# Optimization experiments

Measured on AMD Instinct MI355X. Metric: run time of the kernel, lower is better.

Reference implementation:

```python
import jax, jax.numpy as jnp
import numpy as np

D_MODEL, N_STATE, L_MAX, BATCH = 256, 64, 2048, 16

def _to_c(x):
    return jax.lax.complex(x[..., 0], x[..., 1])

def setup_inputs() -> dict:
    key = jax.random.key(0)
    k_u, k_ct_r, k_ct_i, k_step = jax.random.split(key, 4)
    n, d = N_STATE, D_MODEL
    # --- HiPPO DPLR init (numpy, matches torch hippo_dplr) ---
    P = np.sqrt(1.0 + 2.0 * np.arange(1, n + 1, dtype=np.float64))
    A = np.tril(np.outer(P, P)) - np.diag(np.arange(1, n + 1, dtype=np.float64))
    A = -A
    p = 0.5 * np.sqrt(2.0 * np.arange(1, n + 1, dtype=np.float64) + 1.0)
    Ap = (A + np.outer(p, p)).astype(np.complex64)
    lam, V = np.linalg.eig(Ap)
    p_rot = V.conj().T @ p.astype(np.complex64)
    p_ri = np.stack([p_rot.real, p_rot.imag], -1).astype(np.float32)          # (n,2)
    lambda_ri = np.stack([lam.real, lam.imag], -1).astype(np.float32)         # (n,2)
    # --- B init: sqrt(2k+1), repeated over channels, zero imag ---
    B_r = np.sqrt(2.0 * np.arange(1, n + 1) + 1.0).astype(np.float32)
    B_ri = np.stack([np.tile(B_r, (d, 1)), np.zeros((d, n), np.float32)], -1) # (d,n,2)
    # --- Ct: xavier-normal complex ---
    std = float(np.sqrt(2.0 / (d + n)))
    Ct_r = jax.random.normal(k_ct_r, (d, n), jnp.float32) * (std / np.sqrt(2.0))
    Ct_i = jax.random.normal(k_ct_i, (d, n), jnp.float32) * (std / np.sqrt(2.0))
    Ct_ri = jnp.stack([Ct_r, Ct_i], -1)                                        # (d,n,2)
    Dp = jnp.ones((1, 1, d), jnp.float32)
    log_step = jax.random.uniform(k_step, (d,), jnp.float32) * (
        np.log(0.1) - np.log(0.001)) + np.log(0.001)
    u = jax.random.normal(k_u, (BATCH, L_MAX, d), jnp.float32)
    return {"u": u, "p_ri": jnp.asarray(p_ri), "lambda_ri": jnp.asarray(lambda_ri),
            "B_ri": jnp.asarray(B_ri), "Ct_ri": Ct_ri, "Dp": Dp, "log_step": log_step}

def reference(u, p_ri, lambda_ri, B_ri, Ct_ri, Dp, log_step):
    p = _to_c(p_ri)          # (n,)
    lam = _to_c(lambda_ri)   # (n,)
    B = _to_c(B_ri)          # (d,n)
    Ct = _to_c(Ct_ri)        # (d,n)
    L = u.shape[1]
    omega = jnp.exp(2j * jnp.pi * jnp.arange(L) / L).astype(jnp.complex64)  # (L,)
    step = jnp.exp(log_step)                                               # (d,)
    g = (2.0 / step)[:, None] * ((1.0 - omega) / (1.0 + omega))[None, :]   # (d,L)
    c = 2.0 / (1.0 + omega)                                                # (L,)
    inv = 1.0 / (g[:, :, None] - lam[None, None, :])                       # (d,L,n)
    k00 = jnp.einsum('dn,dln->dl', Ct.conj() * B, inv)
    k01 = jnp.einsum('dn,dln->dl', Ct.conj() * p[None, :], inv)
    k10 = jnp.einsum('dn,dln->dl', p.conj()[None, :] * B, inv)
    k11 = jnp.einsum('n,dln->dl', p.conj() * p, inv)
    at_roots = c[None, :] * (k00 - k01 * k10 / (1.0 + k11))                # (d,L)
    out = jnp.fft.ifft(at_roots, n=L, axis=-1)
    order = jnp.concatenate([jnp.zeros((1,), jnp.int32), jnp.arange(L - 1, 0, -1)])
    K = out[:, order].real[None]                                           # (1,d,L)
    # causal FFT convolution
    ud = jnp.fft.rfft(jnp.pad(u, ((0, 0), (0, L), (0, 0))), axis=1)        # (B,L+1,d)
    Kd = jnp.fft.rfft(jnp.pad(K, ((0, 0), (0, 0), (0, L))), axis=-1)       # (1,d,L+1)
    y = jnp.fft.irfft(jnp.transpose(ud, (0, 2, 1)) * Kd, axis=-1)[..., :L]
    y = jnp.transpose(y, (0, 2, 1)).astype(u.dtype)                        # (B,L,d)
    return y + Dp * u
```

## Files before the change

### kernel.cpp

```cpp
#include <hip/hip_runtime.h>
#include <math.h>

#define LLEN   2048
#define NFFT   4096
#define DMODEL 256
#define NSTATE 64
#define NBATCH 16
#define PI_F   3.14159265358979323846f

#define PADIDX(a) ((a) + ((a) >> 4))
#define LDSN2 (LLEN + (LLEN >> 4))
#define KSTRIDE 2056

#define SWZIDX(a) ((a) ^ (((a) >> 4) & 15))

__device__ inline float frcp(float x) { return __builtin_amdgcn_rcpf(x); }

#define RADIX4(ar0,ai0,ar1,ai1,ar2,ai2,ar3,ai3,S) do {                      \
    float s0r=(ar0)+(ar2), s0i=(ai0)+(ai2);                                 \
    float s1r=(ar0)-(ar2), s1i=(ai0)-(ai2);                                 \
    float s2r=(ar1)+(ar3), s2i=(ai1)+(ai3);                                 \
    float s3r=(ar1)-(ar3), s3i=(ai1)-(ai3);                                 \
    (ar0)=s0r+s2r; (ai0)=s0i+s2i;                                           \
    (ar2)=s0r-s2r; (ai2)=s0i-s2i;                                           \
    (ar1)=s1r-(S)*s3i; (ai1)=s1i+(S)*s3r;                                   \
    (ar3)=s1r+(S)*s3i; (ai3)=s1i-(S)*s3r;                                   \
} while (0)

template<int SIGN>
__device__ inline void dft16_tail(float xr[16], float xi[16]) {
    const float S = (float)SIGN;
    const float C1 = 0.9238795325112867f, S1 = 0.3826834323650898f;
    const float C2 = 0.7071067811865476f;
#define TW(idx, wr_, wi_) { float tr = xr[idx]*(wr_) - xi[idx]*(wi_);       \
    xi[idx] = xr[idx]*(wi_) + xi[idx]*(wr_); xr[idx] = tr; }
    TW(5,  C1,  S*S1);
    TW(6,  C2,  S*C2);
    TW(7,  S1,  S*C1);
    TW(9,  C2,  S*C2);
    TW(10, 0.f, S);
    TW(11, -C2, S*C2);
    TW(13, S1,  S*C1);
    TW(14, -C2, S*C2);
    TW(15, -C1, -S*S1);
#undef TW
    RADIX4(xr[0],xi[0],  xr[1],xi[1],  xr[2],xi[2],  xr[3],xi[3],  S);
    RADIX4(xr[4],xi[4],  xr[5],xi[5],  xr[6],xi[6],  xr[7],xi[7],  S);
    RADIX4(xr[8],xi[8],  xr[9],xi[9],  xr[10],xi[10],xr[11],xi[11],S);
    RADIX4(xr[12],xi[12],xr[13],xi[13],xr[14],xi[14],xr[15],xi[15],S);
}

template<int SIGN>
__device__ inline void dft16(float xr[16], float xi[16]) {
    const float S = (float)SIGN;
    RADIX4(xr[0],xi[0], xr[4],xi[4], xr[8],xi[8],  xr[12],xi[12], S);
    RADIX4(xr[1],xi[1], xr[5],xi[5], xr[9],xi[9],  xr[13],xi[13], S);
    RADIX4(xr[2],xi[2], xr[6],xi[6], xr[10],xi[10],xr[14],xi[14], S);
    RADIX4(xr[3],xi[3], xr[7],xi[7], xr[11],xi[11],xr[15],xi[15], S);
    dft16_tail<SIGN>(xr, xi);
}

template<int SIGN>
__device__ inline void dft16z(float xr[16], float xi[16]) {
    const float S = (float)SIGN;
#define RAD4Z(r0,i0,r1,i1,r2,i2,r3,i3) do {                                 \
    const float a0r=(r0), a0i=(i0), a1r=(r1), a1i=(i1);                     \
    (r0)=a0r+a1r;     (i0)=a0i+a1i;                                         \
    (r2)=a0r-a1r;     (i2)=a0i-a1i;                                         \
    (r1)=a0r-S*a1i;   (i1)=a0i+S*a1r;                                       \
    (r3)=a0r+S*a1i;   (i3)=a0i-S*a1r;                                       \
} while (0)
    RAD4Z(xr[0],xi[0], xr[4],xi[4], xr[8],xi[8],  xr[12],xi[12]);
    RAD4Z(xr[1],xi[1], xr[5],xi[5], xr[9],xi[9],  xr[13],xi[13]);
    RAD4Z(xr[2],xi[2], xr[6],xi[6], xr[10],xi[10],xr[14],xi[14]);
    RAD4Z(xr[3],xi[3], xr[7],xi[7], xr[11],xi[11],xr[15],xi[15]);
#undef RAD4Z
    dft16_tail<SIGN>(xr, xi);
}

template<int SIGN>
__device__ inline void dft8(float xr[8], float xi[8]) {
    const float S = (float)SIGN;
    const float C2 = 0.7071067811865476f;
    RADIX4(xr[0],xi[0], xr[2],xi[2], xr[4],xi[4], xr[6],xi[6], S);
    RADIX4(xr[1],xi[1], xr[3],xi[3], xr[5],xi[5], xr[7],xi[7], S);
    { float tr = xr[3]*C2 - xi[3]*(S*C2); xi[3] = xr[3]*(S*C2) + xi[3]*C2; xr[3] = tr; }
    { float tr = -S*xi[5]; xi[5] = S*xr[5]; xr[5] = tr; }
    { float tr = xr[7]*(-C2) - xi[7]*(S*C2); xi[7] = xr[7]*(S*C2) + xi[7]*(-C2); xr[7] = tr; }
    float br[8], bi[8];
#pragma unroll
    for (int k = 0; k < 4; ++k) {
        br[k]   = xr[2*k] + xr[2*k+1]; bi[k]   = xi[2*k] + xi[2*k+1];
        br[k+4] = xr[2*k] - xr[2*k+1]; bi[k+4] = xi[2*k] - xi[2*k+1];
    }
#pragma unroll
    for (int k = 0; k < 8; ++k) { xr[k] = br[k]; xi[k] = bi[k]; }
}

template<int SIGN>
__device__ inline void tw_apply16(float xr[16], float xi[16], float ang) {
    float wr[16], wi[16];
    __sincosf(ang, &wi[1], &wr[1]);
#pragma unroll
    for (int k = 1; k < 8; ++k) {
        wr[2*k]   = wr[k]*wr[k] - wi[k]*wi[k];
        wi[2*k]   = 2.f * wr[k] * wi[k];
        wr[2*k+1] = wr[k]*wr[k+1] - wi[k]*wi[k+1];
        wi[2*k+1] = wr[k]*wi[k+1] + wi[k]*wr[k+1];
    }
#pragma unroll
    for (int t = 1; t < 16; ++t) {
        float tr = xr[t]*wr[t] - xi[t]*wi[t];
        xi[t] = xr[t]*wi[t] + xi[t]*wr[t];
        xr[t] = tr;
    }
}

template<int SIGN, int M, int L, bool PRUNE>
__device__ inline void stage16(float2* X, int j, bool active) {
    float xr[16], xi[16];
    const int p = j & (L - 1);
    if (active) {
#pragma unroll
        for (int t = 0; t < 16; ++t) {
            float2 v = X[PADIDX(j + t * M)];
            xr[t] = v.x; xi[t] = v.y;
        }
        tw_apply16<SIGN>(xr, xi, ((float)SIGN * 2.f * PI_F / (float)(16 * L)) * (float)p);
        dft16<SIGN>(xr, xi);
    }
    __syncthreads();
    if (active) {
        const int base = 16 * j - 15 * p;
#pragma unroll
        for (int k0 = 0; k0 < 4; ++k0)
#pragma unroll
            for (int k2 = 0; k2 < 4; ++k2) {
                const int u = k0 + 4 * k2;
                if (!PRUNE || u < 8) {
                    const int a = base + u * L;
                    X[PADIDX(a)] = make_float2(xr[4*k0+k2], xi[4*k0+k2]);
                }
            }
    }
    __syncthreads();
}

template<int SIGN>
__device__ inline void fft2048_f2(float2* X, int tid) {
    float xr[8], xi[8];
#pragma unroll
    for (int t = 0; t < 8; ++t) {
        float2 v = X[PADIDX(tid + t * 256)];
        xr[t] = v.x; xi[t] = v.y;
    }
    dft8<SIGN>(xr, xi);
    __syncthreads();
#pragma unroll
    for (int u = 0; u < 8; ++u)
        X[PADIDX(8 * tid + u)] = make_float2(xr[u], xi[u]);
    __syncthreads();
    stage16<SIGN, 128, 8,   false>(X, tid, tid < 128);
    stage16<SIGN, 128, 128, false>(X, tid, tid < 128);
}

template<int SIGN, int M, int L, bool PRUNE>
__device__ inline void stage16s(float2* X, int j) {
    float xr[16], xi[16];
    const int p = j & (L - 1);
#pragma unroll
    for (int t = 0; t < 16; ++t) {
        float2 v = X[SWZIDX(j + t * M)];
        xr[t] = v.x; xi[t] = v.y;
    }
    tw_apply16<SIGN>(xr, xi, ((float)SIGN * 2.f * PI_F / (float)(16 * L)) * (float)p);
    dft16<SIGN>(xr, xi);
    __syncthreads();
    const int base = 16 * j - 15 * p;
#pragma unroll
    for (int k0 = 0; k0 < 4; ++k0)
#pragma unroll
        for (int k2 = 0; k2 < 4; ++k2) {
            const int u = k0 + 4 * k2;
            if (!PRUNE || u < 8) {
                const int a = base + u * L;
                X[SWZIDX(a)] = make_float2(xr[4*k0+k2], xi[4*k0+k2]);
            }
        }
    __syncthreads();
}

template<int SIGN, bool PRUNE>
__device__ inline void fft4096_swz_from_regs(float2* X, int tid,
                                             float xr[16], float xi[16]) {
    dft16z<SIGN>(xr, xi);
#pragma unroll
    for (int k0 = 0; k0 < 4; ++k0)
#pragma unroll
        for (int k2 = 0; k2 < 4; ++k2)
            X[SWZIDX(16 * tid + k0 + 4 * k2)] = make_float2(xr[4*k0+k2], xi[4*k0+k2]);
    __syncthreads();
    stage16s<SIGN, 256, 16,  false>(X, tid);
    stage16s<SIGN, 256, 256, PRUNE>(X, tid);
}

template<int SIGN, bool PRUNE>
__device__ inline void fft4096_swz(float2* X, int tid) {
    float xr[16], xi[16];
#pragma unroll
    for (int t = 0; t < 16; ++t) {
        float2 v = X[SWZIDX(tid + t * 256)];
        xr[t] = v.x; xi[t] = v.y;
    }
    dft16<SIGN>(xr, xi);
    __syncthreads();
#pragma unroll
    for (int k0 = 0; k0 < 4; ++k0)
#pragma unroll
        for (int k2 = 0; k2 < 4; ++k2)
            X[SWZIDX(16 * tid + k0 + 4 * k2)] = make_float2(xr[4*k0+k2], xi[4*k0+k2]);
    __syncthreads();
    stage16s<SIGN, 256, 16,  false>(X, tid);
    stage16s<SIGN, 256, 256, PRUNE>(X, tid);
}

__global__ __launch_bounds__(256) void k_ar(const float* __restrict__ p_ri,
                                            const float* __restrict__ lambda_ri,
                                            const float* __restrict__ B_ri,
                                            const float* __restrict__ Ct_ri,
                                            const float* __restrict__ log_step,
                                            float2* __restrict__ ar_out) {
    __shared__ float4 c0[NSTATE], c1[NSTATE];
    __shared__ float2 lam[NSTATE];
    const int d = blockIdx.x >> 1;
    const int lbase = (blockIdx.x & 1) << 10;
    const int tid = threadIdx.x;
    if (tid < NSTATE) {
        const int n = tid;
        const float px = p_ri[2*n], py = p_ri[2*n+1];
        lam[n] = make_float2(lambda_ri[2*n], lambda_ri[2*n+1]);
        const float Bx = B_ri[(d*NSTATE+n)*2], By = B_ri[(d*NSTATE+n)*2+1];
        const float Cx = Ct_ri[(d*NSTATE+n)*2], Cy = Ct_ri[(d*NSTATE+n)*2+1];
        c0[n] = make_float4(Cx*Bx + Cy*By, Cx*By - Cy*Bx,
                            Cx*px + Cy*py, Cx*py - Cy*px);
        c1[n] = make_float4(px*Bx + py*By, px*By - py*Bx, px*px + py*py, 0.f);
    }
    __syncthreads();

    const float tos = 2.f * __expf(-log_step[d]);
    float gx[4], gy[4], ccx[4], ccy[4];
    float k00x[4], k00y[4], k01x[4], k01y[4];
    float k10x[4], k10y[4], k11x[4], k11y[4];
#pragma unroll
    for (int j = 0; j < 4; ++j) {
        const int l = lbase + tid + (j << 8);
        float sn, cs;
        sincosf(2.f * PI_F * (float)l / (float)LLEN, &sn, &cs);
        const float opx = 1.f + cs, opy = sn;
        const float omx = 1.f - cs, omy = -sn;
        const float inv_op = frcp(opx*opx + opy*opy);
        gx[j] = tos * (omx*opx + omy*opy) * inv_op;
        gy[j] = tos * (omy*opx - omx*opy) * inv_op;
        ccx[j] = 2.f * opx * inv_op; ccy[j] = -2.f * opy * inv_op;
        k00x[j]=0.f; k00y[j]=0.f; k01x[j]=0.f; k01y[j]=0.f;
        k10x[j]=0.f; k10y[j]=0.f; k11x[j]=0.f; k11y[j]=0.f;
    }
    for (int n = 0; n < NSTATE; ++n) {
        const float2 lm = lam[n];
        const float4 a = c0[n];
        const float4 b = c1[n];
#pragma unroll
        for (int j = 0; j < 4; ++j) {
            const float dx = gx[j] - lm.x, dy = gy[j] - lm.y;
            const float idn = frcp(dx*dx + dy*dy);
            const float ix = dx * idn, iy = -dy * idn;
            k00x[j] += a.x*ix - a.y*iy;  k00y[j] += a.x*iy + a.y*ix;
            k01x[j] += a.z*ix - a.w*iy;  k01y[j] += a.z*iy + a.w*ix;
            k10x[j] += b.x*ix - b.y*iy;  k10y[j] += b.x*iy + b.y*ix;
            k11x[j] += b.z*ix;           k11y[j] += b.z*iy;
        }
    }
#pragma unroll
    for (int j = 0; j < 4; ++j) {
        const float nx = k01x[j]*k10x[j] - k01y[j]*k10y[j];
        const float ny = k01x[j]*k10y[j] + k01y[j]*k10x[j];
        const float dpx = 1.f + k11x[j], dpy = k11y[j];
        const float idq = frcp(dpx*dpx + dpy*dpy);
        const float qx = (nx*dpx + ny*dpy) * idq;
        const float qy = (ny*dpx - nx*dpy) * idq;
        const float rx = k00x[j] - qx, ry = k00y[j] - qy;
        ar_out[(size_t)d * LLEN + lbase + tid + (j << 8)] =
            make_float2(ccx[j]*rx - ccy[j]*ry, ccx[j]*ry + ccy[j]*rx);
    }
}

__global__ __launch_bounds__(256, 4) void k_mix(const float* __restrict__ u,
                                                const float2* __restrict__ a_in,
                                                float* __restrict__ ut,
                                                float2* __restrict__ Hc) {
    __shared__ float2 X[LDSN2];
    const int tid = threadIdx.x;

    if (blockIdx.x >= DMODEL) {
        const int blk = blockIdx.x - DMODEL;
        const int bt0 = (blk & 511) * 64;
        const int ch0 = (blk >> 9) * 64;
        float* tile = (float*)X;
        const int tx4 = (tid & 15) * 4;
        const int ty  = tid >> 4;
#pragma unroll
        for (int k = 0; k < 4; ++k) {
            const int r = ty + 16 * k;
            const float4 v = *(const float4*)&u[(size_t)(bt0 + r) * DMODEL + ch0 + tx4];
            tile[r * 65 + tx4 + 0] = v.x;
            tile[r * 65 + tx4 + 1] = v.y;
            tile[r * 65 + tx4 + 2] = v.z;
            tile[r * 65 + tx4 + 3] = v.w;
        }
        __syncthreads();
#pragma unroll
        for (int k = 0; k < 4; ++k) {
            const int c = ty + 16 * k;
            float4 o;
            o.x = tile[(tx4 + 0) * 65 + c];
            o.y = tile[(tx4 + 1) * 65 + c];
            o.z = tile[(tx4 + 2) * 65 + c];
            o.w = tile[(tx4 + 3) * 65 + c];
            *(float4*)&ut[(size_t)(ch0 + c) * (NBATCH * LLEN) + bt0 + tx4] = o;
        }
        return;
    }

    const int d = blockIdx.x;
    const float isc = 1.f / (float)NFFT;
    const float4* a4 = (const float4*)(a_in + (size_t)d * LLEN);
#pragma unroll
    for (int k = 0; k < 4; ++k) {
        const int v = tid + k * 256;
        const float4 w = a4[v];
        X[PADIDX(2 * v)]     = make_float2(w.x, w.y);
        X[PADIDX(2 * v + 1)] = make_float2(w.z, w.w);
    }
    __syncthreads();

    float2* H = Hc + (size_t)d * KSTRIDE;
    for (int m = tid; m <= 1024; m += 256) {
        const float2 am = X[PADIDX(m)];
        const float2 an = X[PADIDX((LLEN - m) & (LLEN - 1))];
        H[2 * m] = make_float2((an.x + am.x) * 0.5f * isc,
                               (an.y - am.y) * 0.5f * isc);
    }
    fft2048_f2<-1>(X, tid);

#pragma unroll
    for (int k = 0; k < 8; ++k) {
        const int j = tid + k * 256;
        const int q = PADIDX(j);
        const float Kj = X[q].x * (1.f / (float)LLEN);
        float snj, csj;
        __sincosf(-PI_F * (float)j * (1.f / 2048.f), &snj, &csj);
        X[q] = make_float2(Kj * csj, Kj * snj);
    }
    __syncthreads();
    fft2048_f2<-1>(X, tid);

    for (int m = tid; m < 1024; m += 256) {
        const float2 w = X[PADIDX(m)];
        H[2 * m + 1] = make_float2(w.x * isc, w.y * isc);
    }
}

__global__ __launch_bounds__(256, 4) void k_conv(const float* __restrict__ ut,
                                                 const float2* __restrict__ Hc,
                                                 const float* __restrict__ Dp,
                                                 float* __restrict__ yt) {
    __shared__ float2 X[NFFT];
    const int bid = blockIdx.x;
    const int x = bid & 7;
    const int s = bid >> 3;
    const int ch = (x << 5) | (s & 31);
    const int pair = s >> 5;
    const int tid = threadIdx.x;

    const float* u0 = ut + (size_t)ch * (NBATCH * LLEN) + (size_t)(2 * pair) * LLEN;
    const float* u1 = u0 + LLEN;

    float xr[16], xi[16];
#pragma unroll
    for (int k = 0; k < 8; ++k) {
        xr[k] = u0[tid + k * 256];
        xi[k] = u1[tid + k * 256];
    }

    fft4096_swz_from_regs<-1, false>(X, tid, xr, xi);

    const float2* H = Hc + (size_t)ch * KSTRIDE;
    for (int f = tid; f <= NFFT / 2; f += 256) {
        const int fb = (NFFT - f) & (NFFT - 1);
        const float2 Za = X[SWZIDX(f)], Zb = X[SWZIDX(fb)];
        const float u0x = 0.5f * (Za.x + Zb.x), u0y = 0.5f * (Za.y - Zb.y);
        const float u1x = 0.5f * (Za.y + Zb.y), u1y = -0.5f * (Za.x - Zb.x);
        const float2 Ha = H[f];
        const float y0x = u0x*Ha.x - u0y*Ha.y, y0y = u0x*Ha.y + u0y*Ha.x;
        const float y1x = u1x*Ha.x - u1y*Ha.y, y1y = u1x*Ha.y + u1y*Ha.x;
        X[SWZIDX(f)] = make_float2(y0x - y1y, y0y + y1x);
        if (fb != f) {
            const float Hbx = Ha.x, Hby = -Ha.y;
            const float z0x = u0x*Hbx + u0y*Hby, z0y = u0x*Hby - u0y*Hbx;
            const float z1x = u1x*Hbx + u1y*Hby, z1y = u1x*Hby - u1y*Hbx;
            X[SWZIDX(fb)] = make_float2(z0x - z1y, z0y + z1x);
        }
    }
    __syncthreads();
    fft4096_swz<+1, true>(X, tid);

    const float dp = Dp[ch];
    float* y0o = yt + (size_t)ch * (NBATCH * LLEN) + (size_t)(2 * pair) * LLEN;
    float* y1o = y0o + LLEN;
#pragma unroll
    for (int k = 0; k < 2; ++k) {
        const int i0 = 4 * (tid + k * 256);
        const float2 va = X[SWZIDX(i0 + 0)];
        const float2 vb = X[SWZIDX(i0 + 1)];
        const float2 vc = X[SWZIDX(i0 + 2)];
        const float2 vd = X[SWZIDX(i0 + 3)];
        const float4 u0v = *(const float4*)&u0[i0];
        const float4 u1v = *(const float4*)&u1[i0];
        float4 o0, o1;
        o0.x = va.x + dp * u0v.x; o0.y = vb.x + dp * u0v.y;
        o0.z = vc.x + dp * u0v.z; o0.w = vd.x + dp * u0v.w;
        o1.x = va.y + dp * u1v.x; o1.y = vb.y + dp * u1v.y;
        o1.z = vc.y + dp * u1v.z; o1.w = vd.y + dp * u1v.w;
        *(float4*)&y0o[i0] = o0;
        *(float4*)&y1o[i0] = o1;
    }
}

__global__ __launch_bounds__(256) void k_post(const float* __restrict__ yt,
                                              float* __restrict__ out) {
    __shared__ float tile[64 * 65];
    const int bt0 = (blockIdx.x & 511) * 64;
    const int ch0 = (blockIdx.x >> 9) * 64;
    const int tid = threadIdx.x;
    const int tx4 = (tid & 15) * 4;
    const int ty  = tid >> 4;
#pragma unroll
    for (int k = 0; k < 4; ++k) {
        const int r = ty + 16 * k;
        const float4 v = *(const float4*)&yt[(size_t)(ch0 + r) * (NBATCH * LLEN) + bt0 + tx4];
        tile[r * 65 + tx4 + 0] = v.x;
        tile[r * 65 + tx4 + 1] = v.y;
        tile[r * 65 + tx4 + 2] = v.z;
        tile[r * 65 + tx4 + 3] = v.w;
    }
    __syncthreads();
#pragma unroll
    for (int k = 0; k < 4; ++k) {
        const int b = ty + 16 * k;
        float4 o;
        o.x = tile[(tx4 + 0) * 65 + b];
        o.y = tile[(tx4 + 1) * 65 + b];
        o.z = tile[(tx4 + 2) * 65 + b];
        o.w = tile[(tx4 + 3) * 65 + b];
        *(float4*)&out[(size_t)(bt0 + b) * DMODEL + ch0 + tx4] = o;
    }
}

extern "C" void kernel_launch(void* const* d_in, const int* in_sizes, int n_in,
                              void* d_out, int out_size, void* d_ws, size_t ws_size,
                              hipStream_t stream) {
    const float* u         = (const float*)d_in[0];
    const float* p_ri      = (const float*)d_in[1];
    const float* lambda_ri = (const float*)d_in[2];
    const float* B_ri      = (const float*)d_in[3];
    const float* Ct_ri     = (const float*)d_in[4];
    const float* Dp        = (const float*)d_in[5];
    const float* log_step  = (const float*)d_in[6];
    float* out = (float*)d_out;

    float2* Hc = (float2*)d_ws;
    char*   wb = (char*)d_ws + (size_t)DMODEL * KSTRIDE * sizeof(float2);
    float2* a  = (float2*)wb;
    float*  yt = (float*)wb;
    float*  ut = out;

    k_ar  <<<DMODEL * 2, 256, 0, stream>>>(p_ri, lambda_ri, B_ri, Ct_ri, log_step, a);
    k_mix <<<DMODEL + 2048, 256, 0, stream>>>(u, a, ut, Hc);
    k_conv<<<DMODEL * (NBATCH / 2), 256, 0, stream>>>(ut, Hc, Dp, yt);
    k_post<<<2048, 256, 0, stream>>>(yt, out);
}
```

Before: 171.5 us.

## Precompute FFT twiddle table and regroup transpose with kernel-coefficient launch

The k_conv FFT stages now read precomputed twiddle factors from a global table instead of doing a sincos plus a multiply chain per stage. One extra block in a new combined pre-kernel builds that table. The u transpose moves out of k_mix into the same pre-kernel alongside the coefficient computation, so it runs concurrently with k_ar's work, and k_mixH handles only the H FFT. The cost is extra global/L2 loads for the twiddles and a larger combined first kernel.

```diff
diff --git a/kernel.cpp b/kernel.cpp
--- a/kernel.cpp
+++ b/kernel.cpp
@@ -11,6 +11,7 @@
 #define PADIDX(a) ((a) + ((a) >> 4))
 #define LDSN2 (LLEN + (LLEN >> 4))
 #define KSTRIDE 2056
+#define TW16OFF (16 * 256)
 
 #define SWZIDX(a) ((a) ^ (((a) >> 4) & 15))
 
@@ -97,10 +98,7 @@
     for (int k = 0; k < 8; ++k) { xr[k] = br[k]; xi[k] = bi[k]; }
 }
 
-template<int SIGN>
-__device__ inline void tw_apply16(float xr[16], float xi[16], float ang) {
-    float wr[16], wi[16];
-    __sincosf(ang, &wi[1], &wr[1]);
+__device__ inline void tw_chain(float wr[16], float wi[16]) {
 #pragma unroll
     for (int k = 1; k < 8; ++k) {
         wr[2*k]   = wr[k]*wr[k] - wi[k]*wi[k];
@@ -108,6 +106,13 @@
         wr[2*k+1] = wr[k]*wr[k+1] - wi[k]*wi[k+1];
         wi[2*k+1] = wr[k]*wi[k+1] + wi[k]*wr[k+1];
     }
+}
+
+template<int SIGN>
+__device__ inline void tw_apply16(float xr[16], float xi[16], float ang) {
+    float wr[16], wi[16];
+    __sincosf(ang, &wi[1], &wr[1]);
+    tw_chain(wr, wi);
 #pragma unroll
     for (int t = 1; t < 16; ++t) {
         float tr = xr[t]*wr[t] - xi[t]*wi[t];
@@ -165,15 +170,26 @@
 }
 
 template<int SIGN, int M, int L, bool PRUNE>
-__device__ inline void stage16s(float2* X, int j) {
+__device__ inline void stage16t(float2* X, int j, const float2* __restrict__ twrow) {
     float xr[16], xi[16];
     const int p = j & (L - 1);
+    float2 w[16];
+#pragma unroll
+    for (int t = 1; t < 16; ++t)
+        w[t] = twrow[t * L + p];
 #pragma unroll
     for (int t = 0; t < 16; ++t) {
         float2 v = X[SWZIDX(j + t * M)];
         xr[t] = v.x; xi[t] = v.y;
     }
-    tw_apply16<SIGN>(xr, xi, ((float)SIGN * 2.f * PI_F / (float)(16 * L)) * (float)p);
+#pragma unroll
+    for (int t = 1; t < 16; ++t) {
+        const float wx = w[t].x;
+        const float wy = (SIGN == -1) ? w[t].y : -w[t].y;
+        const float tr = xr[t]*wx - xi[t]*wy;
+        xi[t] = xr[t]*wy + xi[t]*wx;
+        xr[t] = tr;
+    }
     dft16<SIGN>(xr, xi);
     __syncthreads();
     const int base = 16 * j - 15 * p;
@@ -192,7 +208,8 @@
 
 template<int SIGN, bool PRUNE>
 __device__ inline void fft4096_swz_from_regs(float2* X, int tid,
-                                             float xr[16], float xi[16]) {
+                                             float xr[16], float xi[16],
+                                             const float2* __restrict__ tw) {
     dft16z<SIGN>(xr, xi);
 #pragma unroll
     for (int k0 = 0; k0 < 4; ++k0)
@@ -200,12 +217,13 @@
         for (int k2 = 0; k2 < 4; ++k2)
             X[SWZIDX(16 * tid + k0 + 4 * k2)] = make_float2(xr[4*k0+k2], xi[4*k0+k2]);
     __syncthreads();
-    stage16s<SIGN, 256, 16,  false>(X, tid);
-    stage16s<SIGN, 256, 256, PRUNE>(X, tid);
+    stage16t<SIGN, 256, 16,  false>(X, tid, tw + TW16OFF);
+    stage16t<SIGN, 256, 256, PRUNE>(X, tid, tw);
 }
 
 template<int SIGN, bool PRUNE>
-__device__ inline void fft4096_swz(float2* X, int tid) {
+__device__ inline void fft4096_swz(float2* X, int tid,
+                                   const float2* __restrict__ tw) {
     float xr[16], xi[16];
 #pragma unroll
     for (int t = 0; t < 16; ++t) {
@@ -220,92 +238,94 @@
         for (int k2 = 0; k2 < 4; ++k2)
             X[SWZIDX(16 * tid + k0 + 4 * k2)] = make_float2(xr[4*k0+k2], xi[4*k0+k2]);
     __syncthreads();
-    stage16s<SIGN, 256, 16,  false>(X, tid);
-    stage16s<SIGN, 256, 256, PRUNE>(X, tid);
-}
-
-__global__ __launch_bounds__(256) void k_ar(const float* __restrict__ p_ri,
-                                            const float* __restrict__ lambda_ri,
-                                            const float* __restrict__ B_ri,
-                                            const float* __restrict__ Ct_ri,
-                                            const float* __restrict__ log_step,
-                                            float2* __restrict__ ar_out) {
-    __shared__ float4 c0[NSTATE], c1[NSTATE];
-    __shared__ float2 lam[NSTATE];
-    const int d = blockIdx.x >> 1;
-    const int lbase = (blockIdx.x & 1) << 10;
+    stage16t<SIGN, 256, 16,  false>(X, tid, tw + TW16OFF);
+    stage16t<SIGN, 256, 256, PRUNE>(X, tid, tw);
+}
+
+__global__ __launch_bounds__(256) void k_pre(const float* __restrict__ u,
+                                             const float* __restrict__ p_ri,
+                                             const float* __restrict__ lambda_ri,
+                                             const float* __restrict__ B_ri,
+                                             const float* __restrict__ Ct_ri,
+                                             const float* __restrict__ log_step,
+                                             float2* __restrict__ a_out,
+                                             float* __restrict__ ut,
+                                             float2* __restrict__ tw) {
+    __shared__ float4 shbuf[1040];
+    const int bid = blockIdx.x;
     const int tid = threadIdx.x;
-    if (tid < NSTATE) {
-        const int n = tid;
-        const float px = p_ri[2*n], py = p_ri[2*n+1];
-        lam[n] = make_float2(lambda_ri[2*n], lambda_ri[2*n+1]);
-        const float Bx = B_ri[(d*NSTATE+n)*2], By = B_ri[(d*NSTATE+n)*2+1];
-        const float Cx = Ct_ri[(d*NSTATE+n)*2], Cy = Ct_ri[(d*NSTATE+n)*2+1];
-        c0[n] = make_float4(Cx*Bx + Cy*By, Cx*By - Cy*Bx,
-                            Cx*px + Cy*py, Cx*py - Cy*px);
-        c1[n] = make_float4(px*Bx + py*By, px*By - py*Bx, px*px + py*py, 0.f);
-    }
-    __syncthreads();
-
-    const float tos = 2.f * __expf(-log_step[d]);
-    float gx[4], gy[4], ccx[4], ccy[4];
-    float k00x[4], k00y[4], k01x[4], k01y[4];
-    float k10x[4], k10y[4], k11x[4], k11y[4];
-#pragma unroll
-    for (int j = 0; j < 4; ++j) {
-        const int l = lbase + tid + (j << 8);
-        float sn, cs;
-        sincosf(2.f * PI_F * (float)l / (float)LLEN, &sn, &cs);
-        const float opx = 1.f + cs, opy = sn;
-        const float omx = 1.f - cs, omy = -sn;
-        const float inv_op = frcp(opx*opx + opy*opy);
-        gx[j] = tos * (omx*opx + omy*opy) * inv_op;
-        gy[j] = tos * (omy*opx - omx*opy) * inv_op;
-        ccx[j] = 2.f * opx * inv_op; ccy[j] = -2.f * opy * inv_op;
-        k00x[j]=0.f; k00y[j]=0.f; k01x[j]=0.f; k01y[j]=0.f;
-        k10x[j]=0.f; k10y[j]=0.f; k11x[j]=0.f; k11y[j]=0.f;
-    }
-    for (int n = 0; n < NSTATE; ++n) {
-        const float2 lm = lam[n];
-        const float4 a = c0[n];
-        const float4 b = c1[n];
+
+    if (bid < DMODEL * 2) {
+        float4* c0 = shbuf;
+        float4* c1 = shbuf + 64;
+        float2* lam = (float2*)(shbuf + 128);
+        const int d = bid >> 1;
+        const int lbase = (bid & 1) << 10;
+        if (tid < NSTATE) {
+            const int n = tid;
+            const float px = p_ri[2*n], py = p_ri[2*n+1];
+            lam[n] = make_float2(lambda_ri[2*n], lambda_ri[2*n+1]);
+            const float Bx = B_ri[(d*NSTATE+n)*2], By = B_ri[(d*NSTATE+n)*2+1];
+            const float Cx = Ct_ri[(d*NSTATE+n)*2], Cy = Ct_ri[(d*NSTATE+n)*2+1];
+            c0[n] = make_float4(Cx*Bx + Cy*By, Cx*By - Cy*Bx,
+                                Cx*px + Cy*py, Cx*py - Cy*px);
+            c1[n] = make_float4(px*Bx + py*By, px*By - py*Bx, px*px + py*py, 0.f);
+        }
+        __syncthreads();
+
+        const float tos = 2.f * __expf(-log_step[d]);
+        float gx[4], gy[4], ccx[4], ccy[4];
+        float k00x[4], k00y[4], k01x[4], k01y[4];
+        float k10x[4], k10y[4], k11x[4], k11y[4];
 #pragma unroll
         for (int j = 0; j < 4; ++j) {
-            const float dx = gx[j] - lm.x, dy = gy[j] - lm.y;
-            const float idn = frcp(dx*dx + dy*dy);
-            const float ix = dx * idn, iy = -dy * idn;
-            k00x[j] += a.x*ix - a.y*iy;  k00y[j] += a.x*iy + a.y*ix;
-            k01x[j] += a.z*ix - a.w*iy;  k01y[j] += a.z*iy + a.w*ix;
-            k10x[j] += b.x*ix - b.y*iy;  k10y[j] += b.x*iy + b.y*ix;
-            k11x[j] += b.z*ix;           k11y[j] += b.z*iy;
-        }
-    }
-#pragma unroll
-    for (int j = 0; j < 4; ++j) {
-        const float nx = k01x[j]*k10x[j] - k01y[j]*k10y[j];
-        const float ny = k01x[j]*k10y[j] + k01y[j]*k10x[j];
-        const float dpx = 1.f + k11x[j], dpy = k11y[j];
-        const float idq = frcp(dpx*dpx + dpy*dpy);
-        const float qx = (nx*dpx + ny*dpy) * idq;
-        const float qy = (ny*dpx - nx*dpy) * idq;
-        const float rx = k00x[j] - qx, ry = k00y[j] - qy;
-        ar_out[(size_t)d * LLEN + lbase + tid + (j << 8)] =
-            make_float2(ccx[j]*rx - ccy[j]*ry, ccx[j]*ry + ccy[j]*rx);
-    }
-}
-
-__global__ __launch_bounds__(256, 4) void k_mix(const float* __restrict__ u,
-                                                const float2* __restrict__ a_in,
-                                                float* __restrict__ ut,
-                                                float2* __restrict__ Hc) {
-    __shared__ float2 X[LDSN2];
-    const int tid = threadIdx.x;
-
-    if (blockIdx.x >= DMODEL) {
-        const int blk = blockIdx.x - DMODEL;
+            const int l = lbase + tid + (j << 8);
+            float sn, cs;
+            sincosf(2.f * PI_F * (float)l / (float)LLEN, &sn, &cs);
+            const float opx = 1.f + cs, opy = sn;
+            const float omx = 1.f - cs, omy = -sn;
+            const float inv_op = frcp(opx*opx + opy*opy);
+            gx[j] = tos * (omx*opx + omy*opy) * inv_op;
+            gy[j] = tos * (omy*opx - omx*opy) * inv_op;
+            ccx[j] = 2.f * opx * inv_op; ccy[j] = -2.f * opy * inv_op;
+            k00x[j]=0.f; k00y[j]=0.f; k01x[j]=0.f; k01y[j]=0.f;
+            k10x[j]=0.f; k10y[j]=0.f; k11x[j]=0.f; k11y[j]=0.f;
+        }
+        for (int n = 0; n < NSTATE; ++n) {
+            const float2 lm = lam[n];
+            const float4 a = c0[n];
+            const float4 b = c1[n];
+#pragma unroll
+            for (int j = 0; j < 4; ++j) {
+                const float dx = gx[j] - lm.x, dy = gy[j] - lm.y;
+                const float idn = frcp(dx*dx + dy*dy);
+                const float ix = dx * idn, iy = -dy * idn;
+                k00x[j] += a.x*ix - a.y*iy;  k00y[j] += a.x*iy + a.y*ix;
+                k01x[j] += a.z*ix - a.w*iy;  k01y[j] += a.z*iy + a.w*ix;
+                k10x[j] += b.x*ix - b.y*iy;  k10y[j] += b.x*iy + b.y*ix;
+                k11x[j] += b.z*ix;           k11y[j] += b.z*iy;
+            }
+        }
+#pragma unroll
+        for (int j = 0; j < 4; ++j) {
+            const float nx = k01x[j]*k10x[j] - k01y[j]*k10y[j];
+            const float ny = k01x[j]*k10y[j] + k01y[j]*k10x[j];
+            const float dpx = 1.f + k11x[j], dpy = k11y[j];
+            const float idq = frcp(dpx*dpx + dpy*dpy);
+            const float qx = (nx*dpx + ny*dpy) * idq;
+            const float qy = (ny*dpx - nx*dpy) * idq;
+            const float rx = k00x[j] - qx, ry = k00y[j] - qy;
+            a_out[(size_t)d * LLEN + lbase + tid + (j << 8)] =
+                make_float2(ccx[j]*rx - ccy[j]*ry, ccx[j]*ry + ccy[j]*rx);
+        }
+        return;
+    }
+
+    if (bid < DMODEL * 2 + 2048) {
+        const int blk = bid - DMODEL * 2;
         const int bt0 = (blk & 511) * 64;
         const int ch0 = (blk >> 9) * 64;
-        float* tile = (float*)X;
+        float* tile = (float*)shbuf;
         const int tx4 = (tid & 15) * 4;
         const int ty  = tid >> 4;
 #pragma unroll
@@ -331,6 +351,27 @@
         return;
     }
 
+    {
+        float wr[16], wi[16];
+        __sincosf(-2.f * PI_F * (float)tid * (1.f / 4096.f), &wi[1], &wr[1]);
+        tw_chain(wr, wi);
+#pragma unroll
+        for (int t = 1; t < 16; ++t)
+            tw[t * 256 + tid] = make_float2(wr[t], wi[t]);
+        if (tid < 16) {
+            __sincosf(-2.f * PI_F * (float)tid * (1.f / 256.f), &wi[1], &wr[1]);
+            tw_chain(wr, wi);
+#pragma unroll
+            for (int t = 1; t < 16; ++t)
+                tw[TW16OFF + t * 16 + tid] = make_float2(wr[t], wi[t]);
+        }
+    }
+}
+
+__global__ __launch_bounds__(256, 4) void k_mixH(const float2* __restrict__ a_in,
+                                                 float2* __restrict__ Hc) {
+    __shared__ float2 X[LDSN2];
+    const int tid = threadIdx.x;
     const int d = blockIdx.x;
     const float isc = 1.f / (float)NFFT;
     const float4* a4 = (const float4*)(a_in + (size_t)d * LLEN);
@@ -373,6 +414,7 @@
 __global__ __launch_bounds__(256, 4) void k_conv(const float* __restrict__ ut,
                                                  const float2* __restrict__ Hc,
                                                  const float* __restrict__ Dp,
+                                                 const float2* __restrict__ tw,
                                                  float* __restrict__ yt) {
     __shared__ float2 X[NFFT];
     const int bid = blockIdx.x;
@@ -392,7 +434,7 @@
         xi[k] = u1[tid + k * 256];
     }
 
-    fft4096_swz_from_regs<-1, false>(X, tid, xr, xi);
+    fft4096_swz_from_regs<-1, false>(X, tid, xr, xi, tw);
 
     const float2* H = Hc + (size_t)ch * KSTRIDE;
     for (int f = tid; f <= NFFT / 2; f += 256) {
@@ -412,7 +454,7 @@
         }
     }
     __syncthreads();
-    fft4096_swz<+1, true>(X, tid);
+    fft4096_swz<+1, true>(X, tid, tw);
 
     const float dp = Dp[ch];
     float* y0o = yt + (size_t)ch * (NBATCH * LLEN) + (size_t)(2 * pair) * LLEN;
@@ -482,10 +524,12 @@
     char*   wb = (char*)d_ws + (size_t)DMODEL * KSTRIDE * sizeof(float2);
     float2* a  = (float2*)wb;
     float*  yt = (float*)wb;
+    float2* tw = (float2*)(wb + (size_t)DMODEL * NBATCH * LLEN * sizeof(float));
     float*  ut = out;
 
-    k_ar  <<<DMODEL * 2, 256, 0, stream>>>(p_ri, lambda_ri, B_ri, Ct_ri, log_step, a);
-    k_mix <<<DMODEL + 2048, 256, 0, stream>>>(u, a, ut, Hc);
-    k_conv<<<DMODEL * (NBATCH / 2), 256, 0, stream>>>(ut, Hc, Dp, yt);
+    k_pre <<<DMODEL * 2 + 2048 + 1, 256, 0, stream>>>(u, p_ri, lambda_ri, B_ri,
+                                                      Ct_ri, log_step, a, ut, tw);
+    k_mixH<<<DMODEL, 256, 0, stream>>>(a, Hc);
+    k_conv<<<DMODEL * (NBATCH / 2), 256, 0, stream>>>(ut, Hc, Dp, tw, yt);
     k_post<<<2048, 256, 0, stream>>>(yt, out);
 }
```

After: 186.3 us. 1.09x slower.
